# Kernel optimization log

Hardware: AMD Instinct MI355X
Metric: run time of the kernel (lower is better)

Reference implementation:

```python
import jax, jax.numpy as jnp
import numpy as np


def setup_inputs() -> dict:
    key = jax.random.key(0)
    kq, kk, kv, km = jax.random.split(key, 4)
    B, H, S, D = 2, 16, 2048, 64
    Q = jax.random.normal(kq, (B, H, S, D), dtype=jnp.float32)
    K = jax.random.normal(kk, (B, H, S, D), dtype=jnp.float32)
    V = jax.random.normal(kv, (B, H, S, D), dtype=jnp.float32)
    attn_mask = jax.random.randint(km, (B, 1, S, S), 0, 2).astype(jnp.bool_)
    return {"Q": Q, "K": K, "V": V, "attn_mask": attn_mask}


def reference(Q, K, V, attn_mask):
    d_k = Q.shape[-1]
    # scores = Q @ K^T / sqrt(d_k)  -> [B, H, S, S]
    scores = jnp.einsum('bhqd,bhkd->bhqk', Q, K) / jnp.sqrt(jnp.float32(d_k))
    # faithful to torch masked_fill_(attn_mask, 1e-9): masked positions set to 1e-9
    scores = jnp.where(attn_mask, jnp.float32(1e-9), scores)
    attn = jax.nn.softmax(scores, axis=-1)
    context = jnp.einsum('bhqk,bhkd->bhqd', attn, V)
    return (context, attn)
```

## Files before the change

### kernel.cpp

```cpp
#include <hip/hip_runtime.h>

#define BB 2
#define HH 16
#define SS 2048
#define DD 64

typedef __attribute__((ext_vector_type(8))) _Float16 half8;
typedef __attribute__((ext_vector_type(4))) float f32x4;

__device__ __forceinline__ half8 cvt8(f32x4 a, f32x4 b) {
  half8 r;
  r[0] = (_Float16)a[0]; r[1] = (_Float16)a[1];
  r[2] = (_Float16)a[2]; r[3] = (_Float16)a[3];
  r[4] = (_Float16)b[0]; r[5] = (_Float16)b[1];
  r[6] = (_Float16)b[2]; r[7] = (_Float16)b[3];
  return r;
}

__global__ __launch_bounds__(256, 2)
void sdpa_kernel(const float* __restrict__ Q, const float* __restrict__ K,
                 const float* __restrict__ V, const void* __restrict__ M,
                 float* __restrict__ out_ctx, float* __restrict__ out_attn) {
  __shared__ _Float16 E[16 * 2048];

  const int bh   = blockIdx.y;
  const int b    = bh >> 4;
  const int q0   = blockIdx.x << 4;
  const int tid  = threadIdx.x;
  const int wave = tid >> 6;
  const int lane = tid & 63;
  const int col  = lane & 15;
  const int quad = lane >> 4;

  const unsigned int* mw = (const unsigned int*)M;
  unsigned int probe = mw[lane];
  unsigned long long bi = __ballot(probe <= 1u);
  unsigned long long bf = __ballot(probe == 0u || probe == 0x3f800000u);
  const int mmode = (bi == ~0ull) ? 0 : ((bf == ~0ull) ? 1 : 2);
  const int*           m32 = (const int*)M           + (size_t)b * SS * SS;
  const float*         mfp = (const float*)M         + (size_t)b * SS * SS;
  const unsigned char* m8  = (const unsigned char*)M + (size_t)b * SS * SS;

  const float* Qb = Q + (size_t)bh * SS * DD;
  const float* Kb = K + (size_t)bh * SS * DD;
  const float* Vb = V + (size_t)bh * SS * DD;

  half8 aQ0, aQ1;
  {
    const float* qp = Qb + (size_t)(q0 + col) * DD + quad * 8;
    f32x4 x0 = *(const f32x4*)(qp);
    f32x4 x1 = *(const f32x4*)(qp + 4);
    f32x4 x2 = *(const f32x4*)(qp + 32);
    f32x4 x3 = *(const f32x4*)(qp + 36);
    aQ0 = cvt8(x0, x1);
    aQ1 = cvt8(x2, x3);
  }

  for (int n0 = wave * 16; n0 < SS; n0 += 64) {
    const float* kp = Kb + (size_t)(n0 + col) * DD + quad * 8;
    f32x4 x0 = *(const f32x4*)(kp);
    f32x4 x1 = *(const f32x4*)(kp + 4);
    f32x4 x2 = *(const f32x4*)(kp + 32);
    f32x4 x3 = *(const f32x4*)(kp + 36);
    half8 bK0 = cvt8(x0, x1);
    half8 bK1 = cvt8(x2, x3);
    f32x4 c = {0.f, 0.f, 0.f, 0.f};
    c = __builtin_amdgcn_mfma_f32_16x16x32_f16(aQ0, bK0, c, 0, 0, 0);
    c = __builtin_amdgcn_mfma_f32_16x16x32_f16(aQ1, bK1, c, 0, 0, 0);
    const int key = n0 + col;
#pragma unroll
    for (int r = 0; r < 4; ++r) {
      const int row = quad * 4 + r;
      const size_t midx = (size_t)(q0 + row) * SS + key;
      int mv;
      if (mmode == 0)      mv = m32[midx];
      else if (mmode == 1) mv = (mfp[midx] != 0.f);
      else                 mv = m8[midx];
      const float sc = mv ? 1e-9f : c[r] * 0.125f;
      const float e  = __expf(sc);
      const int gp = (key >> 3) ^ (row & 7);
      E[row * 2048 + gp * 8 + (key & 7)] = (_Float16)e;
    }
  }
  __syncthreads();

#pragma unroll
  for (int r = 0; r < 4; ++r) {
    const int row = wave * 4 + r;
    half8 vals[4];
    float zsum = 0.f;
#pragma unroll
    for (int i = 0; i < 4; ++i) {
      const int gpr = i * 64 + lane;
      vals[i] = *(const half8*)&E[row * 2048 + gpr * 8];
#pragma unroll
      for (int j = 0; j < 8; ++j) zsum += (float)vals[i][j];
    }
#pragma unroll
    for (int off = 1; off < 64; off <<= 1) zsum += __shfl_xor(zsum, off, 64);
    const float rz = 1.0f / zsum;

    float* arow = out_attn + ((size_t)bh * SS + (q0 + row)) * SS;
#pragma unroll
    for (int i = 0; i < 4; ++i) {
      const int gcol = i * 64 + (lane ^ (row & 7));
      f32x4 w0, w1;
      half8 nv;
#pragma unroll
      for (int j = 0; j < 4; ++j) {
        const float p0 = (float)vals[i][j] * rz;
        const float p1 = (float)vals[i][j + 4] * rz;
        w0[j] = p0; w1[j] = p1;
        nv[j] = (_Float16)p0; nv[j + 4] = (_Float16)p1;
      }
      *(f32x4*)(arow + gcol * 8)     = w0;
      *(f32x4*)(arow + gcol * 8 + 4) = w1;
      *(half8*)&E[row * 2048 + (i * 64 + lane) * 8] = nv;
    }
  }
  __syncthreads();

  const int d0 = wave * 16;
  f32x4 u = {0.f, 0.f, 0.f, 0.f};
  for (int kk0 = 0; kk0 < SS; kk0 += 32) {
    const int gp = ((kk0 + quad * 8) >> 3) ^ (col & 7);
    half8 aP = *(const half8*)&E[col * 2048 + gp * 8];
    const float* vp = Vb + (size_t)(kk0 + quad * 8) * DD + d0 + col;
    half8 bV;
#pragma unroll
    for (int jj = 0; jj < 8; ++jj) bV[jj] = (_Float16)vp[(size_t)jj * DD];
    u = __builtin_amdgcn_mfma_f32_16x16x32_f16(aP, bV, u, 0, 0, 0);
  }
#pragma unroll
  for (int r = 0; r < 4; ++r) {
    const int row = quad * 4 + r;
    out_ctx[((size_t)bh * SS + (q0 + row)) * DD + d0 + col] = u[r];
  }
}

extern "C" void kernel_launch(void* const* d_in, const int* in_sizes, int n_in,
                              void* d_out, int out_size, void* d_ws, size_t ws_size,
                              hipStream_t stream) {
  const float* Q = (const float*)d_in[0];
  const float* K = (const float*)d_in[1];
  const float* V = (const float*)d_in[2];
  const void*  M = d_in[3];
  float* ctx  = (float*)d_out;
  float* attn = ctx + (size_t)BB * HH * SS * DD;
  dim3 grid(SS / 16, BB * HH);
  sdpa_kernel<<<grid, 256, 0, stream>>>(Q, K, V, M, ctx, attn);
}
```

Before: 1.184 ms.

## Use 512 threads, accumulate row sums in registers, normalize context after PV

Doubles the block to 8 waves. Row sums of exp are now accumulated in registers during the score pass and reduced through shared memory, which removes the separate full pass that re-read E to sum it. The PV product now runs on the unnormalized fp16 exponentials, split into two key halves across waves and combined via shared scratch, and the result is divided by the row sum at the end. The attention matrix is written last with nontemporal stores. This trades an extra sync and a small reduction step for more parallelism and fewer LDS passes; PV precision shifts slightly because the unnormalized values are used in fp16.

Result: faster. 1.047 ms (-11.6%).

```diff
diff --git a/kernel.cpp b/kernel.cpp
--- a/kernel.cpp
+++ b/kernel.cpp
@@ -17,11 +17,13 @@
   return r;
 }
 
-__global__ __launch_bounds__(256, 2)
+__global__ __launch_bounds__(512, 4)
 void sdpa_kernel(const float* __restrict__ Q, const float* __restrict__ K,
                  const float* __restrict__ V, const void* __restrict__ M,
                  float* __restrict__ out_ctx, float* __restrict__ out_attn) {
   __shared__ _Float16 E[16 * 2048];
+  __shared__ float zacc[8][16];
+  __shared__ f32x4 pscr[4][64];
 
   const int bh   = blockIdx.y;
   const int b    = bh >> 4;
@@ -56,7 +58,9 @@
     aQ1 = cvt8(x2, x3);
   }
 
-  for (int n0 = wave * 16; n0 < SS; n0 += 64) {
+  float zpart[4] = {0.f, 0.f, 0.f, 0.f};
+#pragma unroll 2
+  for (int n0 = wave * 16; n0 < SS; n0 += 128) {
     const float* kp = Kb + (size_t)(n0 + col) * DD + quad * 8;
     f32x4 x0 = *(const f32x4*)(kp);
     f32x4 x1 = *(const f32x4*)(kp + 4);
@@ -78,51 +82,29 @@
       else                 mv = m8[midx];
       const float sc = mv ? 1e-9f : c[r] * 0.125f;
       const float e  = __expf(sc);
+      zpart[r] += e;
       const int gp = (key >> 3) ^ (row & 7);
       E[row * 2048 + gp * 8 + (key & 7)] = (_Float16)e;
     }
   }
-  __syncthreads();
-
 #pragma unroll
   for (int r = 0; r < 4; ++r) {
-    const int row = wave * 4 + r;
-    half8 vals[4];
-    float zsum = 0.f;
-#pragma unroll
-    for (int i = 0; i < 4; ++i) {
-      const int gpr = i * 64 + lane;
-      vals[i] = *(const half8*)&E[row * 2048 + gpr * 8];
-#pragma unroll
-      for (int j = 0; j < 8; ++j) zsum += (float)vals[i][j];
-    }
-#pragma unroll
-    for (int off = 1; off < 64; off <<= 1) zsum += __shfl_xor(zsum, off, 64);
-    const float rz = 1.0f / zsum;
-
-    float* arow = out_attn + ((size_t)bh * SS + (q0 + row)) * SS;
-#pragma unroll
-    for (int i = 0; i < 4; ++i) {
-      const int gcol = i * 64 + (lane ^ (row & 7));
-      f32x4 w0, w1;
-      half8 nv;
-#pragma unroll
-      for (int j = 0; j < 4; ++j) {
-        const float p0 = (float)vals[i][j] * rz;
-        const float p1 = (float)vals[i][j + 4] * rz;
-        w0[j] = p0; w1[j] = p1;
-        nv[j] = (_Float16)p0; nv[j + 4] = (_Float16)p1;
-      }
-      *(f32x4*)(arow + gcol * 8)     = w0;
-      *(f32x4*)(arow + gcol * 8 + 4) = w1;
-      *(half8*)&E[row * 2048 + (i * 64 + lane) * 8] = nv;
-    }
+    float z = zpart[r];
+    z += __shfl_xor(z, 1, 64);
+    z += __shfl_xor(z, 2, 64);
+    z += __shfl_xor(z, 4, 64);
+    z += __shfl_xor(z, 8, 64);
+    if (col == 0) zacc[wave][quad * 4 + r] = z;
   }
   __syncthreads();
 
-  const int d0 = wave * 16;
+  const int d0 = (wave & 3) << 4;
+  const int h  = wave >> 2;
+  const int kbase = h << 10;
   f32x4 u = {0.f, 0.f, 0.f, 0.f};
-  for (int kk0 = 0; kk0 < SS; kk0 += 32) {
+#pragma unroll 2
+  for (int kk = 0; kk < 1024; kk += 32) {
+    const int kk0 = kbase + kk;
     const int gp = ((kk0 + quad * 8) >> 3) ^ (col & 7);
     half8 aP = *(const half8*)&E[col * 2048 + gp * 8];
     const float* vp = Vb + (size_t)(kk0 + quad * 8) * DD + d0 + col;
@@ -131,10 +113,43 @@
     for (int jj = 0; jj < 8; ++jj) bV[jj] = (_Float16)vp[(size_t)jj * DD];
     u = __builtin_amdgcn_mfma_f32_16x16x32_f16(aP, bV, u, 0, 0, 0);
   }
+  if (h) pscr[wave & 3][lane] = u;
+  __syncthreads();
+
+  if (h == 0) {
+    f32x4 u2 = pscr[wave][lane];
 #pragma unroll
-  for (int r = 0; r < 4; ++r) {
-    const int row = quad * 4 + r;
-    out_ctx[((size_t)bh * SS + (q0 + row)) * DD + d0 + col] = u[r];
+    for (int r = 0; r < 4; ++r) {
+      const int row = quad * 4 + r;
+      float z = 0.f;
+#pragma unroll
+      for (int w = 0; w < 8; ++w) z += zacc[w][row];
+      out_ctx[((size_t)bh * SS + (q0 + row)) * DD + d0 + col] = (u[r] + u2[r]) / z;
+    }
+  }
+
+#pragma unroll
+  for (int rr = 0; rr < 2; ++rr) {
+    const int row = (wave << 1) + rr;
+    float z = 0.f;
+#pragma unroll
+    for (int w = 0; w < 8; ++w) z += zacc[w][row];
+    const float rz = 1.0f / z;
+    float* arow = out_attn + ((size_t)bh * SS + (q0 + row)) * SS;
+#pragma unroll
+    for (int i = 0; i < 4; ++i) {
+      const int gpr = i * 64 + lane;
+      half8 v = *(const half8*)&E[row * 2048 + gpr * 8];
+      const int gcol = i * 64 + (lane ^ (row & 7));
+      f32x4 w0, w1;
+#pragma unroll
+      for (int j = 0; j < 4; ++j) {
+        w0[j] = (float)v[j] * rz;
+        w1[j] = (float)v[j + 4] * rz;
+      }
+      __builtin_nontemporal_store(w0, (f32x4*)(arow + gcol * 8));
+      __builtin_nontemporal_store(w1, (f32x4*)(arow + gcol * 8 + 4));
+    }
   }
 }
 
@@ -148,5 +163,5 @@
   float* ctx  = (float*)d_out;
   float* attn = ctx + (size_t)BB * HH * SS * DD;
   dim3 grid(SS / 16, BB * HH);
-  sdpa_kernel<<<grid, 256, 0, stream>>>(Q, K, V, M, ctx, attn);
+  sdpa_kernel<<<grid, 512, 0, stream>>>(Q, K, V, M, ctx, attn);
 }
```
